# Kernel optimization log

Hardware: AMD Instinct MI355X
Metric: run time of the kernel (lower is better)

## Reference

```python
import jax, jax.numpy as jnp
import numpy as np

IN_CH = 4          # qubits
KSZ = 3            # kernel size
NUM_KERNELS = 2
LAYERS = 1
STRIDE = 1
DILATION = 1
NPOS = KSZ * KSZ
TOTAL_W = NPOS * LAYERS * IN_CH * 3  # 108


def setup_inputs() -> dict:
    key = jax.random.key(0)
    k1, k2 = jax.random.split(key)
    x = jax.random.normal(k1, (16, IN_CH, 64, 64), dtype=jnp.float32)
    weights = jax.random.uniform(k2, (NUM_KERNELS, TOTAL_W), minval=-np.pi, maxval=np.pi, dtype=jnp.float32)
    return {"x": x, "weights": weights}


def _apply_1q(state, U, q):
    # state: (N, 2,...,2) with IN_CH qubit axes; U: (2,2) shared or (N,2,2) batched
    s = jnp.moveaxis(state, q + 1, -1)
    if U.ndim == 2:
        s = jnp.einsum('ab,...b->...a', U, s)
    else:
        s = jnp.einsum('nab,n...b->n...a', U, s)
    return jnp.moveaxis(s, -1, q + 1)


def _ry_mat(theta):
    c = jnp.cos(theta / 2)
    s = jnp.sin(theta / 2)
    return jnp.stack([jnp.stack([c, -s], -1), jnp.stack([s, c], -1)], -2).astype(jnp.complex64)


def _rx_mat(theta):
    c = jnp.cos(theta / 2).astype(jnp.complex64)
    s = (-1j) * jnp.sin(theta / 2).astype(jnp.complex64)
    return jnp.stack([jnp.stack([c, s], -1), jnp.stack([s, c], -1)], -2)


def _rz_mat(theta):
    e = jnp.exp((-0.5j) * theta.astype(jnp.complex64))
    z = jnp.zeros_like(e)
    return jnp.stack([jnp.stack([e, z], -1), jnp.stack([z, jnp.conj(e)], -1)], -2)


def _cx(state, cq, tq):
    s = jnp.moveaxis(state, (cq + 1, tq + 1), (-2, -1))
    s = s.at[..., 1, :].set(s[..., 1, ::-1])  # flip target where control=1
    return jnp.moveaxis(s, (-2, -1), (cq + 1, tq + 1))


def _circuit(w_flat, patches):
    # patches: (N, IN_CH, NPOS) data angles; w_flat: (TOTAL_W,)
    n = IN_CH
    N = patches.shape[0]
    dim = 2 ** n
    # H on every qubit from |0...0> == uniform superposition with + amplitudes
    state = jnp.full((N,) + (2,) * n, 1.0 / np.sqrt(dim), dtype=jnp.complex64)
    w = w_flat.reshape(NPOS, LAYERS, n, 3)
    for pos in range(NPOS):
        for ch in range(n):
            state = _apply_1q(state, _ry_mat(patches[:, ch, pos]), ch)
        for l in range(LAYERS):
            for q in range(n):
                state = _apply_1q(state, _rx_mat(w[pos, l, q, 0]), q)
                state = _apply_1q(state, _ry_mat(w[pos, l, q, 1]), q)
                state = _apply_1q(state, _rz_mat(w[pos, l, q, 2]), q)
            for q in range(n - 1):
                state = _cx(state, q, q + 1)
            if n > 1:
                state = _cx(state, n - 1, 0)
    p = jnp.abs(state) ** 2  # (N, 2,...,2)
    sign = jnp.array([1.0, -1.0], dtype=jnp.float32)
    exps = []
    for q in range(n):
        sh = [1] * (n + 1)
        sh[q + 1] = 2
        exps.append(jnp.sum(p * sign.reshape(sh), axis=tuple(range(1, n + 1))))
    return jnp.stack(exps, -1)  # (N, n) <Z_q> expectations


def _extract_patches(x):
    B, C, H, W = x.shape
    out_h = (H - (KSZ - 1) * DILATION - 1) // STRIDE + 1
    out_w = (W - (KSZ - 1) * DILATION - 1) // STRIDE + 1
    hh = (jnp.arange(out_h) * STRIDE)[:, None] + jnp.arange(KSZ)[None, :] * DILATION  # (out_h, K)
    ww = (jnp.arange(out_w) * STRIDE)[:, None] + jnp.arange(KSZ)[None, :] * DILATION  # (out_w, K)
    p = x[:, :, hh][:, :, :, :, ww]                  # (B, C, out_h, K, out_w, K)
    p = p.transpose(0, 2, 4, 1, 3, 5)                # (B, out_h, out_w, C, K, K)
    return p.reshape(B, out_h * out_w, C, KSZ * KSZ), out_h, out_w


def reference(x, weights):
    B, C, H, W = x.shape
    patches, out_h, out_w = _extract_patches(x)
    flat = patches.reshape(B * out_h * out_w, C, KSZ * KSZ)
    outs = []
    for kidx in range(NUM_KERNELS):
        e = _circuit(weights[kidx], flat)                       # (B*P, C)
        e = e.reshape(B, out_h, out_w, C).transpose(0, 3, 1, 2)  # (B, C, out_h, out_w)
        outs.append(e)
    return jnp.concatenate(outs, axis=1)  # (B, NUM_KERNELS*C, out_h, out_w)
```

## Files before the change

### kernel.cpp

```cpp
#include <hip/hip_runtime.h>
#include <math.h>

#define IN_CH 4
#define KSZ 3
#define NUM_KERNELS 2
#define NPOS 9
#define HH 64
#define WW 64
#define BB 16
#define OH 62
#define OW 62
#define NPATCH (BB*OH*OW)
#define NU (NPOS*IN_CH)
#define UFLOATS (NU*8)
#define BLK 64

__global__ void qk_precompute(const float* __restrict__ w, float* __restrict__ U) {
    int t = blockIdx.x * blockDim.x + threadIdx.x;
    if (t >= NUM_KERNELS * NU) return;
    int k   = t / NU;
    int rem = t % NU;
    const float* wp = w + k * (NU * 3) + rem * 3;
    float hx = 0.5f * wp[0], hy = 0.5f * wp[1], hz = 0.5f * wp[2];
    float cx = cosf(hx), sx = sinf(hx);
    float cy = cosf(hy), sy = sinf(hy);
    float cz = cosf(hz), sz = sinf(hz);
    float m00r =  cy * cx, m00i =  sy * sx;
    float m01r = -sy * cx, m01i = -cy * sx;
    float m10r =  sy * cx, m10i = -cy * sx;
    float m11r =  cy * cx, m11i = -sy * sx;
    float* o = U + t * 8;
    o[0] = cz * m00r + sz * m00i;  o[1] = cz * m00i - sz * m00r;
    o[2] = cz * m01r + sz * m01i;  o[3] = cz * m01i - sz * m01r;
    o[4] = cz * m10r - sz * m10i;  o[5] = cz * m10i + sz * m10r;
    o[6] = cz * m11r - sz * m11i;  o[7] = cz * m11i + sz * m11r;
}

__global__ __launch_bounds__(BLK) void qk_main(const float* __restrict__ x,
                                               const float* __restrict__ Uglob,
                                               float* __restrict__ out) {
    __shared__ float sU[UFLOATS];
    const int kidx = blockIdx.y;
    const int tid  = threadIdx.x;
    for (int t = tid; t < UFLOATS; t += BLK) sU[t] = Uglob[kidx * UFLOATS + t];
    __syncthreads();

    int p = blockIdx.x * BLK + tid;
    if (p >= NPATCH) return;
    int b   = p / (OH * OW);
    int rem = p - b * (OH * OW);
    int oh  = rem / OW;
    int ow  = rem - oh * OW;
    const float* xb = x + b * (IN_CH * HH * WW) + oh * WW + ow;

    float xv[NPOS * IN_CH];
    #pragma unroll
    for (int ch = 0; ch < IN_CH; ++ch)
        #pragma unroll
        for (int kh = 0; kh < KSZ; ++kh)
            #pragma unroll
            for (int kw = 0; kw < KSZ; ++kw)
                xv[(kh * KSZ + kw) * IN_CH + ch] = xb[ch * (HH * WW) + kh * WW + kw];

    float sr[16], si[16];
    #pragma unroll
    for (int i = 0; i < 16; ++i) { sr[i] = 0.25f; si[i] = 0.0f; }

    #pragma unroll
    for (int pos = 0; pos < NPOS; ++pos) {
        #pragma unroll
        for (int q = 0; q < IN_CH; ++q) {
            float s, c;
            __sincosf(0.5f * xv[pos * IN_CH + q], &s, &c);
            const float* u = &sU[(pos * IN_CH + q) * 8];
            const float u00r = u[0], u00i = u[1], u01r = u[2], u01i = u[3];
            const float u10r = u[4], u10i = u[5], u11r = u[6], u11i = u[7];
            const float f00r = c * u00r + s * u01r, f00i = c * u00i + s * u01i;
            const float f10r = c * u10r + s * u11r, f10i = c * u10i + s * u11i;
            const float f01r = c * u01r - s * u00r, f01i = c * u01i - s * u00i;
            const float f11r = c * u11r - s * u10r, f11i = c * u11i - s * u10i;
            const int mask = 8 >> q;
            #pragma unroll
            for (int i = 0; i < 16; ++i) {
                if (i & mask) continue;
                const int j = i | mask;
                float ar = sr[i], ai = si[i], br = sr[j], bi = si[j];
                sr[i] = f00r * ar - f00i * ai + f01r * br - f01i * bi;
                si[i] = f00r * ai + f00i * ar + f01r * bi + f01i * br;
                sr[j] = f10r * ar - f10i * ai + f11r * br - f11i * bi;
                si[j] = f10r * ai + f10i * ar + f11r * bi + f11i * br;
            }
        }
        #pragma unroll
        for (int e = 0; e < 4; ++e) {
            const int cmask = 8 >> e;
            const int tmask = 8 >> ((e + 1) & 3);
            #pragma unroll
            for (int i = 0; i < 16; ++i) {
                if ((i & cmask) && !(i & tmask)) {
                    const int j = i | tmask;
                    float tr = sr[i]; sr[i] = sr[j]; sr[j] = tr;
                    float ti = si[i]; si[i] = si[j]; si[j] = ti;
                }
            }
        }
    }

    float p2[16];
    #pragma unroll
    for (int i = 0; i < 16; ++i) p2[i] = sr[i] * sr[i] + si[i] * si[i];

    float* ob = out + ((size_t)(b * (NUM_KERNELS * IN_CH) + kidx * IN_CH) * OH + oh) * OW + ow;
    #pragma unroll
    for (int q = 0; q < IN_CH; ++q) {
        const int mask = 8 >> q;
        float e = 0.0f;
        #pragma unroll
        for (int i = 0; i < 16; ++i) e += (i & mask) ? -p2[i] : p2[i];
        ob[q * (OH * OW)] = e;
    }
}

extern "C" void kernel_launch(void* const* d_in, const int* in_sizes, int n_in,
                              void* d_out, int out_size, void* d_ws, size_t ws_size,
                              hipStream_t stream) {
    const float* x = (const float*)d_in[0];
    const float* w = (const float*)d_in[1];
    float* out = (float*)d_out;
    float* U   = (float*)d_ws;

    hipLaunchKernelGGL(qk_precompute, dim3(1), dim3(128), 0, stream, w, U);
    dim3 grid((NPATCH + BLK - 1) / BLK, NUM_KERNELS);
    hipLaunchKernelGGL(qk_main, grid, dim3(BLK), 0, stream, x, U, out);
}
```

Measured before the change: 74.79 us.

## Fuse gate-matrix precompute into main kernel and stream patch loads per position

The separate precompute kernel is removed; each block now builds the 36 fused rotation matrices in shared memory from the weights, which drops one launch and the global round trip. The position loop is no longer unrolled (unroll 1), and input values are loaded per position instead of being preloaded into a 36-entry register array, which lowers register pressure and code size. The bounds check is dropped because NPATCH divides evenly by the block size. The trade-off is redundant trig per block and less load-latency hiding across positions.

```diff
diff --git a/kernel.cpp b/kernel.cpp
--- a/kernel.cpp
+++ b/kernel.cpp
@@ -15,94 +15,85 @@
 #define UFLOATS (NU*8)
 #define BLK 64
 
-__global__ void qk_precompute(const float* __restrict__ w, float* __restrict__ U) {
-    int t = blockIdx.x * blockDim.x + threadIdx.x;
-    if (t >= NUM_KERNELS * NU) return;
-    int k   = t / NU;
-    int rem = t % NU;
-    const float* wp = w + k * (NU * 3) + rem * 3;
-    float hx = 0.5f * wp[0], hy = 0.5f * wp[1], hz = 0.5f * wp[2];
-    float cx = cosf(hx), sx = sinf(hx);
-    float cy = cosf(hy), sy = sinf(hy);
-    float cz = cosf(hz), sz = sinf(hz);
-    float m00r =  cy * cx, m00i =  sy * sx;
-    float m01r = -sy * cx, m01i = -cy * sx;
-    float m10r =  sy * cx, m10i = -cy * sx;
-    float m11r =  cy * cx, m11i = -sy * sx;
-    float* o = U + t * 8;
-    o[0] = cz * m00r + sz * m00i;  o[1] = cz * m00i - sz * m00r;
-    o[2] = cz * m01r + sz * m01i;  o[3] = cz * m01i - sz * m01r;
-    o[4] = cz * m10r - sz * m10i;  o[5] = cz * m10i + sz * m10r;
-    o[6] = cz * m11r - sz * m11i;  o[7] = cz * m11i + sz * m11r;
-}
-
 __global__ __launch_bounds__(BLK) void qk_main(const float* __restrict__ x,
-                                               const float* __restrict__ Uglob,
+                                               const float* __restrict__ w,
                                                float* __restrict__ out) {
     __shared__ float sU[UFLOATS];
     const int kidx = blockIdx.y;
     const int tid  = threadIdx.x;
-    for (int t = tid; t < UFLOATS; t += BLK) sU[t] = Uglob[kidx * UFLOATS + t];
+
+    if (tid < NU) {
+        const float* wp = w + kidx * (NU * 3) + tid * 3;
+        float hx = 0.5f * wp[0], hy = 0.5f * wp[1], hz = 0.5f * wp[2];
+        float cx = cosf(hx), sx = sinf(hx);
+        float cy = cosf(hy), sy = sinf(hy);
+        float cz = cosf(hz), sz = sinf(hz);
+        float m00r =  cy * cx, m00i =  sy * sx;
+        float m01r = -sy * cx, m01i = -cy * sx;
+        float m10r =  sy * cx, m10i = -cy * sx;
+        float m11r =  cy * cx, m11i = -sy * sx;
+        float* o = &sU[tid * 8];
+        o[0] = cz * m00r + sz * m00i;  o[1] = cz * m00i - sz * m00r;
+        o[2] = cz * m01r + sz * m01i;  o[3] = cz * m01i - sz * m01r;
+        o[4] = cz * m10r - sz * m10i;  o[5] = cz * m10i + sz * m10r;
+        o[6] = cz * m11r - sz * m11i;  o[7] = cz * m11i + sz * m11r;
+    }
     __syncthreads();
 
-    int p = blockIdx.x * BLK + tid;
-    if (p >= NPATCH) return;
-    int b   = p / (OH * OW);
-    int rem = p - b * (OH * OW);
-    int oh  = rem / OW;
-    int ow  = rem - oh * OW;
-    const float* xb = x + b * (IN_CH * HH * WW) + oh * WW + ow;
-
-    float xv[NPOS * IN_CH];
-    #pragma unroll
-    for (int ch = 0; ch < IN_CH; ++ch)
-        #pragma unroll
-        for (int kh = 0; kh < KSZ; ++kh)
-            #pragma unroll
-            for (int kw = 0; kw < KSZ; ++kw)
-                xv[(kh * KSZ + kw) * IN_CH + ch] = xb[ch * (HH * WW) + kh * WW + kw];
+    const int p   = blockIdx.x * BLK + tid;
+    const int b   = p / (OH * OW);
+    const int rem = p - b * (OH * OW);
+    const int oh  = rem / OW;
+    const int ow  = rem - oh * OW;
+    const float* xp = x + b * (IN_CH * HH * WW) + oh * WW + ow;
 
     float sr[16], si[16];
     #pragma unroll
     for (int i = 0; i < 16; ++i) { sr[i] = 0.25f; si[i] = 0.0f; }
 
-    #pragma unroll
-    for (int pos = 0; pos < NPOS; ++pos) {
-        #pragma unroll
-        for (int q = 0; q < IN_CH; ++q) {
-            float s, c;
-            __sincosf(0.5f * xv[pos * IN_CH + q], &s, &c);
-            const float* u = &sU[(pos * IN_CH + q) * 8];
-            const float u00r = u[0], u00i = u[1], u01r = u[2], u01i = u[3];
-            const float u10r = u[4], u10i = u[5], u11r = u[6], u11i = u[7];
-            const float f00r = c * u00r + s * u01r, f00i = c * u00i + s * u01i;
-            const float f10r = c * u10r + s * u11r, f10i = c * u10i + s * u11i;
-            const float f01r = c * u01r - s * u00r, f01i = c * u01i - s * u00i;
-            const float f11r = c * u11r - s * u10r, f11i = c * u11i - s * u10i;
-            const int mask = 8 >> q;
+    int ubase = 0;
+    #pragma unroll 1
+    for (int kh = 0; kh < KSZ; ++kh) {
+        #pragma unroll 1
+        for (int kw = 0; kw < KSZ; ++kw) {
+            const float* xq = xp + kh * WW + kw;
             #pragma unroll
-            for (int i = 0; i < 16; ++i) {
-                if (i & mask) continue;
-                const int j = i | mask;
-                float ar = sr[i], ai = si[i], br = sr[j], bi = si[j];
-                sr[i] = f00r * ar - f00i * ai + f01r * br - f01i * bi;
-                si[i] = f00r * ai + f00i * ar + f01r * bi + f01i * br;
-                sr[j] = f10r * ar - f10i * ai + f11r * br - f11i * bi;
-                si[j] = f10r * ai + f10i * ar + f11r * bi + f11i * br;
-            }
-        }
-        #pragma unroll
-        for (int e = 0; e < 4; ++e) {
-            const int cmask = 8 >> e;
-            const int tmask = 8 >> ((e + 1) & 3);
-            #pragma unroll
-            for (int i = 0; i < 16; ++i) {
-                if ((i & cmask) && !(i & tmask)) {
-                    const int j = i | tmask;
-                    float tr = sr[i]; sr[i] = sr[j]; sr[j] = tr;
-                    float ti = si[i]; si[i] = si[j]; si[j] = ti;
+            for (int q = 0; q < IN_CH; ++q) {
+                float s, c;
+                __sincosf(0.5f * xq[q * (HH * WW)], &s, &c);
+                const float* u = &sU[ubase + q * 8];
+                const float u00r = u[0], u00i = u[1], u01r = u[2], u01i = u[3];
+                const float u10r = u[4], u10i = u[5], u11r = u[6], u11i = u[7];
+                const float f00r = c * u00r + s * u01r, f00i = c * u00i + s * u01i;
+                const float f10r = c * u10r + s * u11r, f10i = c * u10i + s * u11i;
+                const float f01r = c * u01r - s * u00r, f01i = c * u01i - s * u00i;
+                const float f11r = c * u11r - s * u10r, f11i = c * u11i - s * u10i;
+                const int mask = 8 >> q;
+                #pragma unroll
+                for (int i = 0; i < 16; ++i) {
+                    if (i & mask) continue;
+                    const int j = i | mask;
+                    float ar = sr[i], ai = si[i], br = sr[j], bi = si[j];
+                    sr[i] = f00r * ar - f00i * ai + f01r * br - f01i * bi;
+                    si[i] = f00r * ai + f00i * ar + f01r * bi + f01i * br;
+                    sr[j] = f10r * ar - f10i * ai + f11r * br - f11i * bi;
+                    si[j] = f10r * ai + f10i * ar + f11r * bi + f11i * br;
                 }
             }
+            #pragma unroll
+            for (int e = 0; e < 4; ++e) {
+                const int cmask = 8 >> e;
+                const int tmask = 8 >> ((e + 1) & 3);
+                #pragma unroll
+                for (int i = 0; i < 16; ++i) {
+                    if ((i & cmask) && !(i & tmask)) {
+                        const int j = i | tmask;
+                        float tr = sr[i]; sr[i] = sr[j]; sr[j] = tr;
+                        float ti = si[i]; si[i] = si[j]; si[j] = ti;
+                    }
+                }
+            }
+            ubase += 32;
         }
     }
 
@@ -127,9 +118,8 @@
     const float* x = (const float*)d_in[0];
     const float* w = (const float*)d_in[1];
     float* out = (float*)d_out;
-    float* U   = (float*)d_ws;
+    (void)d_ws; (void)ws_size;
 
-    hipLaunchKernelGGL(qk_precompute, dim3(1), dim3(128), 0, stream, w, U);
-    dim3 grid((NPATCH + BLK - 1) / BLK, NUM_KERNELS);
-    hipLaunchKernelGGL(qk_main, grid, dim3(BLK), 0, stream, x, U, out);
+    dim3 grid(NPATCH / BLK, NUM_KERNELS);
+    hipLaunchKernelGGL(qk_main, grid, dim3(BLK), 0, stream, x, w, out);
 }
```

After: 82.91 us. +10.8%, slower.
